# Kernel optimization log

Measured on AMD Instinct MI355X. Metric: run time of the kernel, lower is better.

## Reference

```python
import jax, jax.numpy as jnp
import numpy as np

B, S, D_IN = 2, 2048, 1024
D_OUT, H, W = 1024, 16, 256
HD = D_OUT // H
SCALE = 1.0 / np.sqrt(HD).astype(np.float32)


def setup_inputs() -> dict:
    key = jax.random.key(0)
    k1, k2, k3 = jax.random.split(key, 3)
    x = jax.random.normal(k1, (B, S, D_IN), dtype=jnp.float32)
    W_qkv = jax.random.normal(k2, (3 * D_OUT, D_IN), dtype=jnp.float32) * 0.02
    W_out = jax.random.normal(k3, (D_OUT, D_OUT), dtype=jnp.float32) * 0.02
    b_out = jnp.zeros((D_OUT,), dtype=jnp.float32)
    return {"x": x, "W_qkv": W_qkv, "W_out": W_out, "b_out": b_out}


def reference(x, W_qkv, W_out, b_out):
    b, s, _ = x.shape
    qkv = x @ W_qkv.T  # [b, s, 3*D_OUT]
    q, k, v = jnp.split(qkv, 3, axis=-1)
    # [b, h, s, hd]
    q = q.reshape(b, s, H, HD).transpose(0, 2, 1, 3)
    k = k.reshape(b, s, H, HD).transpose(0, 2, 1, 3)
    v = v.reshape(b, s, H, HD).transpose(0, 2, 1, 3)
    scores = jnp.einsum('bhqd,bhkd->bhqk', q, k) * SCALE
    idx = jnp.arange(s)
    mask = jnp.abs(idx[:, None] - idx[None, :]) <= W  # symmetric band
    scores = jnp.where(mask[None, None], scores, -jnp.inf)
    probs = jax.nn.softmax(scores, axis=-1)
    ctx = jnp.einsum('bhqk,bhkd->bhqd', probs, v)
    ctx = ctx.transpose(0, 2, 1, 3).reshape(b, s, D_OUT)
    return ctx @ W_out.T + b_out
```

## Files before the change

kernel.cpp:

```cpp
#include <hip/hip_runtime.h>

#define S_LEN   2048
#define N_HEAD  16
#define WINSZ   256
#define ATT_SCALE 0.125f

typedef short bf16x8 __attribute__((ext_vector_type(8)));
typedef float f32x4  __attribute__((ext_vector_type(4)));

__device__ __forceinline__ unsigned short f2bf(float f) {
    union { float f; unsigned u; } x; x.f = f;
    return (unsigned short)((x.u + 0x7FFFu + ((x.u >> 16) & 1u)) >> 16);
}

__device__ __forceinline__ void gl2lds16(const unsigned short* g, unsigned short* l) {
    __builtin_amdgcn_global_load_lds(
        (const __attribute__((address_space(1))) unsigned int*)g,
        (__attribute__((address_space(3))) unsigned int*)l, 16, 0, 0);
}

__global__ void cvt_all(const float* __restrict__ x, const float* __restrict__ wqkv,
                        const float* __restrict__ wout,
                        unsigned short* __restrict__ xb, unsigned short* __restrict__ wqkvb,
                        unsigned short* __restrict__ woutb) {
    int i = blockIdx.x * 256 + threadIdx.x;
    const float4* src; ushort4* dst; int off;
    if (i < 1048576)              { src = (const float4*)x;    dst = (ushort4*)xb;    off = i; }
    else if (i < 1048576 + 786432){ src = (const float4*)wqkv; dst = (ushort4*)wqkvb; off = i - 1048576; }
    else                          { src = (const float4*)wout; dst = (ushort4*)woutb; off = i - 1835008; }
    float4 v = src[off];
    ushort4 o;
    o.x = f2bf(v.x); o.y = f2bf(v.y); o.z = f2bf(v.z); o.w = f2bf(v.w);
    dst[off] = o;
}

template<int MODE, int BN>
__global__ __launch_bounds__(256, 3)
void gemm_bt(const unsigned short* __restrict__ A, const unsigned short* __restrict__ Bm,
             int K,
             unsigned short* __restrict__ qout, unsigned short* __restrict__ kout,
             unsigned short* __restrict__ vtout,
             float* __restrict__ Cout, const float* __restrict__ bias, int N)
{
    constexpr int NJ = BN / 32;
    __shared__ unsigned short Als[128 * 64];
    __shared__ unsigned short Bls[BN * 64];

    const int tid   = threadIdx.x;
    const int lane  = tid & 63;
    const int wave  = tid >> 6;
    const int bm    = blockIdx.y, bn = blockIdx.x;
    const int wm    = (wave >> 1) * 64;
    const int wn    = (wave & 1) * (BN / 2);
    const int col16 = lane & 15;
    const int quad  = lane >> 4;

    f32x4 acc[4][NJ];
#pragma unroll
    for (int i = 0; i < 4; ++i)
#pragma unroll
        for (int j = 0; j < NJ; ++j)
            acc[i][j] = f32x4{0.f, 0.f, 0.f, 0.f};

    const int    grow     = lane >> 3;
    const int    gchk     = (lane & 7) ^ grow;
    const size_t laneoff  = (size_t)grow * K + gchk * 8;
    const unsigned short* gA = A  + (size_t)(bm * 128) * K + laneoff;
    const unsigned short* gB = Bm + (size_t)(bn * BN)  * K + laneoff;

    for (int k0 = 0; k0 < K; k0 += 64) {
        __syncthreads();
#pragma unroll
        for (int i = 0; i < 4; ++i) {
            const int r0 = wave * 32 + i * 8;
            gl2lds16(gA + (size_t)r0 * K + k0, &Als[r0 * 64]);
        }
#pragma unroll
        for (int i = 0; i < BN / 32; ++i) {
            const int r0 = wave * (BN / 4) + i * 8;
            gl2lds16(gB + (size_t)r0 * K + k0, &Bls[r0 * 64]);
        }
        __syncthreads();

#pragma unroll
        for (int kc = 0; kc < 2; ++kc) {
            bf16x8 af[4], bfr[NJ];
            const int sw = (kc * 4 + quad) ^ (col16 & 7);
#pragma unroll
            for (int i = 0; i < 4; ++i)
                af[i]  = *(const bf16x8*)(&Als[(wm + i * 16 + col16) * 64 + sw * 8]);
#pragma unroll
            for (int j = 0; j < NJ; ++j)
                bfr[j] = *(const bf16x8*)(&Bls[(wn + j * 16 + col16) * 64 + sw * 8]);
#pragma unroll
            for (int i = 0; i < 4; ++i)
#pragma unroll
                for (int j = 0; j < NJ; ++j)
                    acc[i][j] = __builtin_amdgcn_mfma_f32_16x16x32_bf16(af[i], bfr[j], acc[i][j], 0, 0, 0);
        }
    }

    if (MODE == 0) {
        const int which = bn >> 3;
#pragma unroll
        for (int i = 0; i < 4; ++i)
#pragma unroll
            for (int j = 0; j < NJ; ++j)
#pragma unroll
                for (int r = 0; r < 4; ++r) {
                    int m = bm * 128 + wm + i * 16 + quad * 4 + r;
                    int n = bn * BN  + wn + j * 16 + col16;
                    int rem = n & 1023;
                    int h = rem >> 6, d = rem & 63;
                    int b = m >> 11, s = m & 2047;
                    unsigned short bv = f2bf(acc[i][j][r]);
                    if (which == 0)
                        qout[((size_t)(b * N_HEAD + h) * S_LEN + s) * 64 + d] = bv;
                    else if (which == 1)
                        kout[((size_t)(b * N_HEAD + h) * S_LEN + s) * 64 + d] = bv;
                    else
                        vtout[((size_t)(b * N_HEAD + h) * 64 + d) * S_LEN + s] = bv;
                }
    } else {
#pragma unroll
        for (int i = 0; i < 4; ++i)
#pragma unroll
            for (int j = 0; j < NJ; ++j)
#pragma unroll
                for (int r = 0; r < 4; ++r) {
                    int m = bm * 128 + wm + i * 16 + quad * 4 + r;
                    int n = bn * BN  + wn + j * 16 + col16;
                    Cout[(size_t)m * N + n] = acc[i][j][r] + bias[n];
                }
    }
}

__global__ __launch_bounds__(256, 2)
void attn_kernel(const unsigned short* __restrict__ Qg, const unsigned short* __restrict__ Kg,
                 const unsigned short* __restrict__ Vtg, unsigned short* __restrict__ ctx)
{
    constexpr int LD = 72;
    __shared__ unsigned short Kls[64 * LD];
    __shared__ unsigned short Vls[64 * LD];
    __shared__ unsigned short Pls[4][32 * LD];

    const int tid  = threadIdx.x;
    const int lane = tid & 63;
    const int wave = tid >> 6;
    const int col  = lane & 15;
    const int quad = lane >> 4;

    const int bh  = blockIdx.y;
    const int Q0  = blockIdx.x * 128;
    const int q0w = Q0 + wave * 32;

    const unsigned short* Qb  = Qg  + (size_t)bh * S_LEN * 64;
    const unsigned short* Kb  = Kg  + (size_t)bh * S_LEN * 64;
    const unsigned short* Vtb = Vtg + (size_t)bh * 64 * S_LEN;

    bf16x8 qa[2][2];
#pragma unroll
    for (int qf = 0; qf < 2; ++qf)
#pragma unroll
        for (int kc = 0; kc < 2; ++kc)
            qa[qf][kc] = *(const bf16x8*)(Qb + (size_t)(q0w + qf * 16 + col) * 64 + kc * 32 + quad * 8);

    f32x4 acc[2][4];
    float lsum[2][4];
#pragma unroll
    for (int qf = 0; qf < 2; ++qf)
#pragma unroll
        for (int d = 0; d < 4; ++d) {
            acc[qf][d] = f32x4{0.f, 0.f, 0.f, 0.f};
            lsum[qf][d] = 0.f;
        }

    const int srow = tid >> 2;
    const int scg  = tid & 3;

    for (int c = 0; c < 10; ++c) {
        const int kb = Q0 - WINSZ + c * 64;
        __syncthreads();
        {
            int kk = kb + srow;
            kk = kk < 0 ? 0 : (kk > S_LEN - 1 ? S_LEN - 1 : kk);
#pragma unroll
            for (int h2 = 0; h2 < 2; ++h2) {
                const int ch = scg * 8 + h2 * 32;
                *(bf16x8*)(&Kls[srow * LD + ch]) = *(const bf16x8*)(Kb + (size_t)kk * 64 + ch);
                int ss = kb + ch;
                ss = ss < 0 ? 0 : (ss > S_LEN - 8 ? S_LEN - 8 : ss);
                *(bf16x8*)(&Vls[srow * LD + ch]) = *(const bf16x8*)(Vtb + (size_t)srow * S_LEN + ss);
            }
        }
        __syncthreads();

        if (kb > q0w + 31 + WINSZ || kb + 63 < q0w - WINSZ || kb > S_LEN - 1 || kb + 63 < 0)
            continue;

        f32x4 sc[2][4];
#pragma unroll
        for (int hf = 0; hf < 4; ++hf) {
            bf16x8 kf0 = *(const bf16x8*)(&Kls[(hf * 16 + col) * LD + quad * 8]);
            bf16x8 kf1 = *(const bf16x8*)(&Kls[(hf * 16 + col) * LD + 32 + quad * 8]);
#pragma unroll
            for (int qf = 0; qf < 2; ++qf) {
                f32x4 z = f32x4{0.f, 0.f, 0.f, 0.f};
                z = __builtin_amdgcn_mfma_f32_16x16x32_bf16(qa[qf][0], kf0, z, 0, 0, 0);
                sc[qf][hf] = __builtin_amdgcn_mfma_f32_16x16x32_bf16(qa[qf][1], kf1, z, 0, 0, 0);
            }
        }

        const bool full = (kb >= q0w + 31 - WINSZ) && (kb + 63 <= q0w + WINSZ) &&
                          (kb >= 0) && (kb + 63 <= S_LEN - 1);

        float p[2][4][4];
#pragma unroll
        for (int qf = 0; qf < 2; ++qf)
#pragma unroll
            for (int hf = 0; hf < 4; ++hf) {
                const int kkey = kb + hf * 16 + col;
#pragma unroll
                for (int r = 0; r < 4; ++r) {
                    float e = __expf(fmaf(sc[qf][hf][r], ATT_SCALE, -8.0f));
                    if (!full) {
                        int q  = q0w + qf * 16 + quad * 4 + r;
                        int dq = kkey - q;
                        bool valid = (kkey >= 0) && (kkey < S_LEN) && (dq <= WINSZ) && (dq >= -WINSZ);
                        e = valid ? e : 0.f;
                    }
                    p[qf][hf][r] = e;
                    lsum[qf][r] += e;
                }
            }

        unsigned short* pw = &Pls[wave][0];
#pragma unroll
        for (int qf = 0; qf < 2; ++qf)
#pragma unroll
            for (int hf = 0; hf < 4; ++hf)
#pragma unroll
                for (int r = 0; r < 4; ++r)
                    pw[(qf * 16 + quad * 4 + r) * LD + hf * 16 + col] = f2bf(p[qf][hf][r]);
        asm volatile("s_waitcnt lgkmcnt(0)" ::: "memory");
        bf16x8 pf[2][2];
#pragma unroll
        for (int qf = 0; qf < 2; ++qf) {
            pf[qf][0] = *(const bf16x8*)(&pw[(qf * 16 + col) * LD + quad * 8]);
            pf[qf][1] = *(const bf16x8*)(&pw[(qf * 16 + col) * LD + 32 + quad * 8]);
        }

#pragma unroll
        for (int d = 0; d < 4; ++d)
#pragma unroll
            for (int kc = 0; kc < 2; ++kc) {
                bf16x8 vf = *(const bf16x8*)(&Vls[(d * 16 + col) * LD + kc * 32 + quad * 8]);
#pragma unroll
                for (int qf = 0; qf < 2; ++qf)
                    acc[qf][d] = __builtin_amdgcn_mfma_f32_16x16x32_bf16(pf[qf][kc], vf, acc[qf][d], 0, 0, 0);
            }
    }

    const int b = bh >> 4, h = bh & 15;
#pragma unroll
    for (int qf = 0; qf < 2; ++qf)
#pragma unroll
        for (int r = 0; r < 4; ++r) {
            float v = lsum[qf][r];
            v += __shfl_xor(v, 1);
            v += __shfl_xor(v, 2);
            v += __shfl_xor(v, 4);
            v += __shfl_xor(v, 8);
            float inv = 1.f / v;
            int q = q0w + qf * 16 + quad * 4 + r;
#pragma unroll
            for (int d = 0; d < 4; ++d)
                ctx[((size_t)(b * S_LEN + q)) * 1024 + h * 64 + d * 16 + col] =
                    f2bf(acc[qf][d][r] * inv);
        }
}

extern "C" void kernel_launch(void* const* d_in, const int* in_sizes, int n_in,
                              void* d_out, int out_size, void* d_ws, size_t ws_size,
                              hipStream_t stream) {
    const float* x    = (const float*)d_in[0];
    const float* Wqkv = (const float*)d_in[1];
    const float* Wout = (const float*)d_in[2];
    const float* bout = (const float*)d_in[3];
    float* out = (float*)d_out;

    char* ws = (char*)d_ws;
    unsigned short* xb    = (unsigned short*)(ws);
    unsigned short* wqkvb = (unsigned short*)(ws + 8u  * 1024 * 1024);
    unsigned short* woutb = (unsigned short*)(ws + 14u * 1024 * 1024);
    unsigned short* qb    = (unsigned short*)(ws + 16u * 1024 * 1024);
    unsigned short* kbuf  = (unsigned short*)(ws + 24u * 1024 * 1024);
    unsigned short* vtbuf = (unsigned short*)(ws + 32u * 1024 * 1024);
    unsigned short* ctxb  = (unsigned short*)(ws + 40u * 1024 * 1024);

    cvt_all<<<8192, 256, 0, stream>>>(x, Wqkv, Wout, xb, wqkvb, woutb);

    gemm_bt<0, 128><<<dim3(24, 32), 256, 0, stream>>>(xb, wqkvb, 1024, qb, kbuf, vtbuf,
                                                      nullptr, nullptr, 0);
    attn_kernel<<<dim3(16, 32), 256, 0, stream>>>(qb, kbuf, vtbuf, ctxb);
    gemm_bt<1, 64><<<dim3(16, 32), 256, 0, stream>>>(ctxb, woutb, 1024, nullptr, nullptr, nullptr,
                                                     out, bout, 1024);
}
```

Before: 166.0 us.

## Widen attention blocks to 256 queries and stage K/V via direct global-to-LDS loads

The attention kernel now runs 8 waves per block, each covering 32 queries, so a block handles 256 queries and loads 12 key/value chunks shared by all waves instead of 10 chunks for 128 queries. This cuts redundant K/V loading relative to the queries served. K/V tiles are copied with global_load_lds into unpadded, XOR-swizzled LDS layouts instead of passing through registers, and the reads are swizzled to match so bank conflicts stay low. The probability rounding switches to a cheaper round-half-up bf16 conversion. The grid halves to 256 blocks, which may lower occupancy and parallelism on a GPU with many CUs.

```diff
diff --git a/kernel.cpp b/kernel.cpp
--- a/kernel.cpp
+++ b/kernel.cpp
@@ -11,6 +11,10 @@
 __device__ __forceinline__ unsigned short f2bf(float f) {
     union { float f; unsigned u; } x; x.f = f;
     return (unsigned short)((x.u + 0x7FFFu + ((x.u >> 16) & 1u)) >> 16);
+}
+__device__ __forceinline__ unsigned short f2bf_rhu(float f) {
+    union { float f; unsigned u; } x; x.f = f;
+    return (unsigned short)((x.u + 0x8000u) >> 16);
 }
 
 __device__ __forceinline__ void gl2lds16(const unsigned short* g, unsigned short* l) {
@@ -135,14 +139,13 @@
     }
 }
 
-__global__ __launch_bounds__(256, 2)
+__global__ __launch_bounds__(512, 2)
 void attn_kernel(const unsigned short* __restrict__ Qg, const unsigned short* __restrict__ Kg,
                  const unsigned short* __restrict__ Vtg, unsigned short* __restrict__ ctx)
 {
-    constexpr int LD = 72;
-    __shared__ unsigned short Kls[64 * LD];
-    __shared__ unsigned short Vls[64 * LD];
-    __shared__ unsigned short Pls[4][32 * LD];
+    __shared__ unsigned short Kls[64 * 64];
+    __shared__ unsigned short Vls[64 * 64];
+    __shared__ unsigned short Pls[8][32 * 72];
 
     const int tid  = threadIdx.x;
     const int lane = tid & 63;
@@ -151,7 +154,7 @@
     const int quad = lane >> 4;
 
     const int bh  = blockIdx.y;
-    const int Q0  = blockIdx.x * 128;
+    const int Q0  = blockIdx.x * 256;
     const int q0w = Q0 + wave * 32;
 
     const unsigned short* Qb  = Qg  + (size_t)bh * S_LEN * 64;
@@ -175,23 +178,21 @@
             lsum[qf][d] = 0.f;
         }
 
-    const int srow = tid >> 2;
-    const int scg  = tid & 3;
-
-    for (int c = 0; c < 10; ++c) {
+    const int rsub = lane >> 3;
+    const int gch  = (lane & 7) ^ rsub;
+    const int swz  = quad;
+
+    for (int c = 0; c < 12; ++c) {
         const int kb = Q0 - WINSZ + c * 64;
         __syncthreads();
         {
-            int kk = kb + srow;
-            kk = kk < 0 ? 0 : (kk > S_LEN - 1 ? S_LEN - 1 : kk);
-#pragma unroll
-            for (int h2 = 0; h2 < 2; ++h2) {
-                const int ch = scg * 8 + h2 * 32;
-                *(bf16x8*)(&Kls[srow * LD + ch]) = *(const bf16x8*)(Kb + (size_t)kk * 64 + ch);
-                int ss = kb + ch;
-                ss = ss < 0 ? 0 : (ss > S_LEN - 8 ? S_LEN - 8 : ss);
-                *(bf16x8*)(&Vls[srow * LD + ch]) = *(const bf16x8*)(Vtb + (size_t)srow * S_LEN + ss);
-            }
+            int krow = kb + wave * 8 + rsub;
+            krow = krow < 0 ? 0 : (krow > S_LEN - 1 ? S_LEN - 1 : krow);
+            gl2lds16(Kb + (size_t)krow * 64 + gch * 8, &Kls[wave * 512]);
+            int drow = wave * 8 + rsub;
+            int ss = kb + gch * 8;
+            ss = ss < 0 ? 0 : (ss > S_LEN - 8 ? S_LEN - 8 : ss);
+            gl2lds16(Vtb + (size_t)drow * S_LEN + ss, &Vls[wave * 512]);
         }
         __syncthreads();
 
@@ -201,8 +202,11 @@
         f32x4 sc[2][4];
 #pragma unroll
         for (int hf = 0; hf < 4; ++hf) {
-            bf16x8 kf0 = *(const bf16x8*)(&Kls[(hf * 16 + col) * LD + quad * 8]);
-            bf16x8 kf1 = *(const bf16x8*)(&Kls[(hf * 16 + col) * LD + 32 + quad * 8]);
+            const int rw = (hf * 16 + col) * 64;
+            const int s0 = ((0 * 4 + swz) ^ (col & 7)) * 8;
+            const int s1 = ((1 * 4 + swz) ^ (col & 7)) * 8;
+            bf16x8 kf0 = *(const bf16x8*)(&Kls[rw + s0]);
+            bf16x8 kf1 = *(const bf16x8*)(&Kls[rw + s1]);
 #pragma unroll
             for (int qf = 0; qf < 2; ++qf) {
                 f32x4 z = f32x4{0.f, 0.f, 0.f, 0.f};
@@ -241,24 +245,27 @@
             for (int hf = 0; hf < 4; ++hf)
 #pragma unroll
                 for (int r = 0; r < 4; ++r)
-                    pw[(qf * 16 + quad * 4 + r) * LD + hf * 16 + col] = f2bf(p[qf][hf][r]);
+                    pw[(qf * 16 + quad * 4 + r) * 72 + hf * 16 + col] = f2bf_rhu(p[qf][hf][r]);
         asm volatile("s_waitcnt lgkmcnt(0)" ::: "memory");
         bf16x8 pf[2][2];
 #pragma unroll
         for (int qf = 0; qf < 2; ++qf) {
-            pf[qf][0] = *(const bf16x8*)(&pw[(qf * 16 + col) * LD + quad * 8]);
-            pf[qf][1] = *(const bf16x8*)(&pw[(qf * 16 + col) * LD + 32 + quad * 8]);
-        }
-
-#pragma unroll
-        for (int d = 0; d < 4; ++d)
+            pf[qf][0] = *(const bf16x8*)(&pw[(qf * 16 + col) * 72 + quad * 8]);
+            pf[qf][1] = *(const bf16x8*)(&pw[(qf * 16 + col) * 72 + 32 + quad * 8]);
+        }
+
+#pragma unroll
+        for (int d = 0; d < 4; ++d) {
+            const int rw = (d * 16 + col) * 64;
 #pragma unroll
             for (int kc = 0; kc < 2; ++kc) {
-                bf16x8 vf = *(const bf16x8*)(&Vls[(d * 16 + col) * LD + kc * 32 + quad * 8]);
+                const int so = ((kc * 4 + swz) ^ (col & 7)) * 8;
+                bf16x8 vf = *(const bf16x8*)(&Vls[rw + so]);
 #pragma unroll
                 for (int qf = 0; qf < 2; ++qf)
                     acc[qf][d] = __builtin_amdgcn_mfma_f32_16x16x32_bf16(pf[qf][kc], vf, acc[qf][d], 0, 0, 0);
             }
+        }
     }
 
     const int b = bh >> 4, h = bh & 15;
@@ -302,7 +309,7 @@
 
     gemm_bt<0, 128><<<dim3(24, 32), 256, 0, stream>>>(xb, wqkvb, 1024, qb, kbuf, vtbuf,
                                                       nullptr, nullptr, 0);
-    attn_kernel<<<dim3(16, 32), 256, 0, stream>>>(qb, kbuf, vtbuf, ctxb);
+    attn_kernel<<<dim3(8, 32), 512, 0, stream>>>(qb, kbuf, vtbuf, ctxb);
     gemm_bt<1, 64><<<dim3(16, 32), 256, 0, stream>>>(ctxb, woutb, 1024, nullptr, nullptr, nullptr,
                                                      out, bout, 1024);
 }
```

After: 163.4 us. About the same (-1.6%).
